# Performance work log

Hardware: AMD Instinct MI355X
Metric: run time of the kernel (lower is better)

Reference implementation:

```python
import jax, jax.numpy as jnp
import numpy as np
from math import sqrt

B, N, CS, H, D, K = 8, 256, 512, 8, 64, 32
NB = 2 * K + 1          # no_bins = 65
CT = 2048               # c_transition
INF = 1e9
WL = sqrt(0.5)          # w_L
EPS = 1e-5


def setup_inputs() -> dict:
    key = jax.random.key(0)
    ks = jax.random.split(key, 10)
    sc = 0.02
    return {
        "s": jax.random.normal(ks[0], (B, N, CS), jnp.float32),
        "masks": jnp.ones((B, N), jnp.bool_),
        "wq": jax.random.normal(ks[1], (CS, D * H), jnp.float32) * sc,
        "wk": jax.random.normal(ks[2], (CS, D * H), jnp.float32) * sc,
        "wv": jax.random.normal(ks[3], (CS, D * H), jnp.float32) * sc,
        "wb": jax.random.normal(ks[4], (NB, H), jnp.float32) * sc,
        "wo": jax.random.normal(ks[5], ((NB + D) * H, CS), jnp.float32) * sc,
        "bo": jnp.zeros((CS,), jnp.float32),
        "ln1_g": jnp.ones((CS,), jnp.float32),
        "ln1_b": jnp.zeros((CS,), jnp.float32),
        "w1": jax.random.normal(ks[6], (CS, CT), jnp.float32) * sc,
        "b1": jnp.zeros((CT,), jnp.float32),
        "w2": jax.random.normal(ks[7], (CT, CS), jnp.float32) * sc,
        "b2": jnp.zeros((CS,), jnp.float32),
        "ln2_g": jnp.ones((CS,), jnp.float32),
        "ln2_b": jnp.zeros((CS,), jnp.float32),
    }


def _layernorm(x, g, b):
    m = jnp.mean(x, -1, keepdims=True)
    v = jnp.var(x, -1, keepdims=True)
    return (x - m) * jax.lax.rsqrt(v + EPS) * g + b


def _heads(x):  # [B,N,D*H] -> [B,H,N,D]  (torch: reshape(B,N,D,H) then move H forward)
    return jnp.transpose(x.reshape(B, N, D, H), (0, 3, 1, 2))


def reference(s, masks, wq, wk, wv, wb, wo, bo, ln1_g, ln1_b, w1, b1, w2, b2, ln2_g, ln2_b):
    mf = masks.astype(s.dtype)                       # [B,N]
    sq = mf[:, :, None] * mf[:, None, :]             # [B,N,N]

    # relative position one-hot, clipped to [-K, K] -> [N,N,NB]
    r = jnp.arange(N)
    dmat = jnp.clip(r[:, None] - r[None, :], -K, K) + K
    relpos_base = jax.nn.one_hot(dmat, NB, dtype=s.dtype)
    relpos = relpos_base[None] * sq[..., None]       # [B,N,N,NB]

    b_bias = jnp.einsum('bijc,ch->bhij', relpos, wb)  # [B,H,N,N]

    q = _heads(s @ wq)                               # [B,H,N,D]
    k = _heads(s @ wk)
    v = _heads(s @ wv)

    logits = WL * (jnp.einsum('bhid,bhjd->bhij', q, k) / sqrt(D) + b_bias)
    logits = logits - INF * (1.0 - sq)[:, None]      # mask
    a = jax.nn.softmax(logits, axis=-1)              # [B,H,N,N]

    # pairwise aggregation and value aggregation (einsum avoids [B,H,N,N,NB] blowup)
    o_pair = jnp.einsum('bhij,bijc->bhic', a, relpos)  # [B,H,N,NB]
    o = jnp.einsum('bhij,bhjd->bhid', a, v)            # [B,H,N,D]

    op = jnp.transpose(o_pair, (0, 2, 1, 3)).reshape(B, N, H * NB)
    ov = jnp.transpose(o, (0, 2, 1, 3)).reshape(B, N, H * D)
    embd = jnp.concatenate([op, ov], axis=-1) @ wo + bo   # [B,N,CS]

    x = _layernorm(s + embd, ln1_g, ln1_b)
    ff = jax.nn.relu(x @ w1 + b1) @ w2 + b2
    x = _layernorm(x + ff, ln2_g, ln2_b)
    return x, a
```

## Files before the change

kernel.cpp:

```cpp
#include <hip/hip_runtime.h>
#include <hip/hip_bf16.h>
#include <cstdint>

#define B_ 8
#define N_ 256
#define CS_ 512
#define H_ 8
#define D_ 64
#define K_ 32
#define NB_ 65
#define CT_ 2048
#define WL_ 0.70710678118654752f

typedef __attribute__((ext_vector_type(8))) short bf16x8;
typedef __attribute__((ext_vector_type(4))) float f32x4;

#define GLOBAL_AS __attribute__((address_space(1)))
#define LDS_AS __attribute__((address_space(3)))

__device__ __forceinline__ void async16(void* lds, const void* g) {
  __builtin_amdgcn_global_load_lds((const GLOBAL_AS uint32_t*)g,
                                   (LDS_AS uint32_t*)lds, 16, 0, 0);
}

__device__ __forceinline__ ushort f2bf(float v) {
  __hip_bfloat16 hb = __float2bfloat16(v);
  return *(ushort*)&hb;
}

__device__ __forceinline__ float bf2f(ushort u) {
  union { uint32_t ui; float f; } cv; cv.ui = (uint32_t)u << 16;
  return cv.f;
}

__global__ __launch_bounds__(128, 2) void gemm_bf16(
    const ushort* __restrict__ A, const ushort* __restrict__ Bt,
    const float* __restrict__ bias, float* __restrict__ C,
    ushort* __restrict__ Cb, int M, int Nc, int Kd, int flags) {
  __shared__ ushort As[2][64 * 64];
  __shared__ ushort Bs[2][64 * 64];
  int tid = threadIdx.x;
  int bm = blockIdx.y * 64, bn = blockIdx.x * 64;
  int S = gridDim.z, z = blockIdx.z;
  int T = Kd >> 6;
  int it0 = (z * T) / S, it1 = ((z + 1) * T) / S;
  if (flags & 32) Cb += (size_t)z * M * Nc;
  int w = tid >> 6, l = tid & 63;
  int lm = l & 15, lq = l >> 4;
  int srow = tid >> 3;
  int sg = tid & 7;

  f32x4 acc[2][4];
#pragma unroll
  for (int i = 0; i < 2; ++i)
#pragma unroll
    for (int j = 0; j < 4; ++j) acc[i][j] = (f32x4){0.f, 0.f, 0.f, 0.f};

  {
    int k0 = it0 << 6;
#pragma unroll
    for (int r = 0; r < 4; ++r) {
      int row = r * 16 + srow;
      int gl = sg ^ (row & 7);
      async16(&As[0][row * 64 + sg * 8],
              A + (size_t)(bm + row) * Kd + k0 + gl * 8);
      async16(&Bs[0][row * 64 + sg * 8],
              Bt + (size_t)(bn + row) * Kd + k0 + gl * 8);
    }
  }
  for (int it = it0; it < it1; ++it) {
    int cur = (it - it0) & 1;
    __syncthreads();
    if (it + 1 < it1) {
      int nxt = cur ^ 1;
      int k0 = (it + 1) << 6;
#pragma unroll
      for (int r = 0; r < 4; ++r) {
        int row = r * 16 + srow;
        int gl = sg ^ (row & 7);
        async16(&As[nxt][row * 64 + sg * 8],
                A + (size_t)(bm + row) * Kd + k0 + gl * 8);
        async16(&Bs[nxt][row * 64 + sg * 8],
                Bt + (size_t)(bn + row) * Kd + k0 + gl * 8);
      }
    }
#pragma unroll
    for (int kk = 0; kk < 2; ++kk) {
      bf16x8 af[2], bfr[4];
#pragma unroll
      for (int i = 0; i < 2; ++i) {
        int ma = w * 32 + 16 * i + lm;
        af[i] = *(const bf16x8*)&As[cur][ma * 64 + ((kk * 4 + lq) ^ (ma & 7)) * 8];
      }
#pragma unroll
      for (int j = 0; j < 4; ++j) {
        int nb = 16 * j + lm;
        bfr[j] = *(const bf16x8*)&Bs[cur][nb * 64 + ((kk * 4 + lq) ^ (nb & 7)) * 8];
      }
#pragma unroll
      for (int i = 0; i < 2; ++i)
#pragma unroll
        for (int j = 0; j < 4; ++j)
          acc[i][j] = __builtin_amdgcn_mfma_f32_16x16x32_bf16(
              af[i], bfr[j], acc[i][j], 0, 0, 0);
    }
  }
  __syncthreads();

  int lr = l >> 3, lc = l & 7;
  ushort* Tb = &As[0][0] + w * 2048;

#pragma unroll
  for (int j = 0; j < 4; ++j) {
    float bv = ((flags & 1) && z == 0) ? bias[bn + 16 * j + lm] : 0.f;
#pragma unroll
    for (int i = 0; i < 2; ++i)
#pragma unroll
      for (int r = 0; r < 4; ++r) {
        float v = acc[i][j][r] + bv;
        if (flags & 2) v = fmaxf(v, 0.f);
        Tb[(16 * i + lq * 4 + r) * 64 + 16 * j + lm] = f2bf(v);
      }
  }
  __asm__ __volatile__("" ::: "memory");
#pragma unroll
  for (int p = 0; p < 4; ++p) {
    int rowL = p * 8 + lr;
    bf16x8 vv = *(const bf16x8*)&Tb[rowL * 64 + lc * 8];
    *(bf16x8*)(Cb + (size_t)(bm + w * 32 + rowL) * Nc + bn + lc * 8) = vv;
  }
}

__global__ __launch_bounds__(128, 2) void qkvT(
    const ushort* __restrict__ A, const ushort* __restrict__ Bt,
    ushort* __restrict__ Cb,
    const float* __restrict__ wo, const float* __restrict__ w1,
    const float* __restrict__ w2, ushort* __restrict__ wopT,
    ushort* __restrict__ w1T, ushort* __restrict__ w2T) {
  __shared__ __align__(16) ushort As[2][64 * 64];
  __shared__ ushort Bs[2][64 * 64];
  int blk = blockIdx.x, tid = threadIdx.x;

  if (blk >= 768) {
    float (*tile)[33] = (float(*)[33])&As[0][0];
    int t = blk - 768;
    const float* src; ushort* dst;
    int R, C, Kpad, tX, tIdx;
    if (t < 544)       { tIdx = t;        src = wo; dst = wopT; R = 1032; C = 512;  Kpad = 1088; tX = 16; }
    else if (t < 1568) { tIdx = t - 544;  src = w1; dst = w1T;  R = 512;  C = 2048; Kpad = 512;  tX = 64; }
    else               { tIdx = t - 1568; src = w2; dst = w2T;  R = 2048; C = 512;  Kpad = 2048; tX = 16; }
    int c0 = (tIdx % tX) * 32, r0 = (tIdx / tX) * 32;
    int tx = tid & 7, ty = tid >> 3;
#pragma unroll
    for (int yy = 0; yy < 32; yy += 16) {
      int r = r0 + yy + ty, c = c0 + tx * 4;
      float4 v = (r < R) ? *(const float4*)&src[(size_t)r * C + c]
                         : (float4){0.f, 0.f, 0.f, 0.f};
      tile[yy + ty][tx * 4 + 0] = v.x;
      tile[yy + ty][tx * 4 + 1] = v.y;
      tile[yy + ty][tx * 4 + 2] = v.z;
      tile[yy + ty][tx * 4 + 3] = v.w;
    }
    __syncthreads();
#pragma unroll
    for (int yy = 0; yy < 32; yy += 16) {
      int cc = c0 + yy + ty;
      int k = r0 + tx * 4;
      float a0 = tile[tx * 4 + 0][yy + ty];
      float a1 = tile[tx * 4 + 1][yy + ty];
      float a2 = tile[tx * 4 + 2][yy + ty];
      float a3 = tile[tx * 4 + 3][yy + ty];
      ushort pk[4] = {f2bf(a0), f2bf(a1), f2bf(a2), f2bf(a3)};
      *(uint2*)&dst[(size_t)cc * Kpad + k] = *(uint2*)pk;
    }
    return;
  }

  int bm = (blk / 24) * 64, bn = (blk % 24) * 64;
  const int Kd = 512, it1 = 8;
  int w = tid >> 6, l = tid & 63;
  int lm = l & 15, lq = l >> 4;
  int srow = tid >> 3;
  int sg = tid & 7;

  f32x4 acc[2][4];
#pragma unroll
  for (int i = 0; i < 2; ++i)
#pragma unroll
    for (int j = 0; j < 4; ++j) acc[i][j] = (f32x4){0.f, 0.f, 0.f, 0.f};

  {
#pragma unroll
    for (int r = 0; r < 4; ++r) {
      int row = r * 16 + srow;
      int gl = sg ^ (row & 7);
      async16(&As[0][row * 64 + sg * 8],
              A + (size_t)(bm + row) * Kd + gl * 8);
      async16(&Bs[0][row * 64 + sg * 8],
              Bt + (size_t)(bn + row) * Kd + gl * 8);
    }
  }
  for (int it = 0; it < it1; ++it) {
    int cur = it & 1;
    __syncthreads();
    if (it + 1 < it1) {
      int nxt = cur ^ 1;
      int k0 = (it + 1) << 6;
#pragma unroll
      for (int r = 0; r < 4; ++r) {
        int row = r * 16 + srow;
        int gl = sg ^ (row & 7);
        async16(&As[nxt][row * 64 + sg * 8],
                A + (size_t)(bm + row) * Kd + k0 + gl * 8);
        async16(&Bs[nxt][row * 64 + sg * 8],
                Bt + (size_t)(bn + row) * Kd + k0 + gl * 8);
      }
    }
#pragma unroll
    for (int kk = 0; kk < 2; ++kk) {
      bf16x8 af[2], bfr[4];
#pragma unroll
      for (int i = 0; i < 2; ++i) {
        int ma = w * 32 + 16 * i + lm;
        af[i] = *(const bf16x8*)&As[cur][ma * 64 + ((kk * 4 + lq) ^ (ma & 7)) * 8];
      }
#pragma unroll
      for (int j = 0; j < 4; ++j) {
        int nb = 16 * j + lm;
        bfr[j] = *(const bf16x8*)&Bs[cur][nb * 64 + ((kk * 4 + lq) ^ (nb & 7)) * 8];
      }
#pragma unroll
      for (int i = 0; i < 2; ++i)
#pragma unroll
        for (int j = 0; j < 4; ++j)
          acc[i][j] = __builtin_amdgcn_mfma_f32_16x16x32_bf16(
              af[i], bfr[j], acc[i][j], 0, 0, 0);
    }
  }
  __syncthreads();

  int lr = l >> 3, lc = l & 7;
  ushort* Tb = &As[0][0] + w * 2048;

  int which = bn >> 9;
  int hh = (bn & 511) >> 6;
  int b = bm >> 8, nn0 = bm & 255;
  if (which == 2) {
#pragma unroll
    for (int j = 0; j < 4; ++j)
#pragma unroll
      for (int i = 0; i < 2; ++i) {
        ushort pk[4];
#pragma unroll
        for (int r = 0; r < 4; ++r) pk[r] = f2bf(acc[i][j][r]);
        *(uint2*)&Tb[(16 * j + lm) * 32 + 16 * i + lq * 4] = *(uint2*)pk;
      }
  } else {
#pragma unroll
    for (int j = 0; j < 4; ++j)
#pragma unroll
      for (int i = 0; i < 2; ++i)
#pragma unroll
        for (int r = 0; r < 4; ++r)
          Tb[(16 * i + lq * 4 + r) * 64 + 16 * j + lm] = f2bf(acc[i][j][r]);
  }
  __asm__ __volatile__("" ::: "memory");
  ushort* dstb = Cb + (size_t)which * 1048576 + (size_t)(b * 8 + hh) * 16384;
  if (which == 2) {
    int vr = l >> 2, vc = l & 3;
#pragma unroll
    for (int p = 0; p < 4; ++p) {
      int rowL = p * 16 + vr;
      bf16x8 vv = *(const bf16x8*)&Tb[rowL * 32 + vc * 8];
      *(bf16x8*)(dstb + (size_t)rowL * 256 + nn0 + w * 32 + vc * 8) = vv;
    }
  } else {
#pragma unroll
    for (int p = 0; p < 4; ++p) {
      int rowL = p * 8 + lr;
      bf16x8 vv = *(const bf16x8*)&Tb[rowL * 64 + lc * 8];
      *(bf16x8*)(dstb + (size_t)(nn0 + w * 32 + rowL) * 64 + lc * 8) = vv;
    }
  }
}

__global__ __launch_bounds__(256) void prep_small(
    const float* __restrict__ s, __hip_bfloat16* __restrict__ s_bf,
    const float* __restrict__ wq, const float* __restrict__ wk,
    const float* __restrict__ wv, __hip_bfloat16* __restrict__ wqkvT) {
  int blk = blockIdx.x;
  if (blk < 512) {
    int i = blk * 256 + threadIdx.x;
    float4 a = ((const float4*)s)[i * 2];
    float4 c = ((const float4*)s)[i * 2 + 1];
    ushort pk[8] = {f2bf(a.x), f2bf(a.y), f2bf(a.z), f2bf(a.w),
                    f2bf(c.x), f2bf(c.y), f2bf(c.z), f2bf(c.w)};
    *(uint4*)&((ushort*)s_bf)[i * 8] = *(uint4*)pk;
    return;
  }
  int t = blk - 512;
  __shared__ float tile[32][33];
  int zz = t >> 8, tIdx = t & 255;
  const float* src = zz == 0 ? wq : zz == 1 ? wk : wv;
  int whichBase = zz * 512;
  int c0 = (tIdx & 15) * 32, r0 = (tIdx >> 4) * 32;
  int tx = threadIdx.x & 7, ty = threadIdx.x >> 3;
  {
    int r = r0 + ty, c = c0 + tx * 4;
    float4 v = *(const float4*)&src[(size_t)r * 512 + c];
    tile[ty][tx * 4 + 0] = v.x;
    tile[ty][tx * 4 + 1] = v.y;
    tile[ty][tx * 4 + 2] = v.z;
    tile[ty][tx * 4 + 3] = v.w;
  }
  __syncthreads();
  {
    int cc = c0 + ty;
    int k = r0 + tx * 4;
    float a0 = tile[tx * 4 + 0][ty];
    float a1 = tile[tx * 4 + 1][ty];
    float a2 = tile[tx * 4 + 2][ty];
    float a3 = tile[tx * 4 + 3][ty];
    int n = whichBase + (cc & 7) * 64 + (cc >> 3);
    ushort pk[4] = {f2bf(a0), f2bf(a1), f2bf(a2), f2bf(a3)};
    *(uint2*)&((ushort*)wqkvT)[(size_t)n * 512 + k] = *(uint2*)pk;
  }
}

__global__ __launch_bounds__(128) void attn_fused(
    const ushort* __restrict__ qh, const ushort* __restrict__ kh,
    const ushort* __restrict__ vT, const int* __restrict__ masks,
    const float* __restrict__ wb, float* __restrict__ a_out,
    ushort* __restrict__ cat) {
  int strip = blockIdx.x & 7, bh = blockIdx.x >> 3;
  int h = bh & 7, b = bh >> 3;
  __shared__ ushort Ks[256 * 64];
  __shared__ ushort Ps[32 * 64];
  __shared__ float wbs[NB_];
  __shared__ float mfj[256];
  int tid = threadIdx.x;
  int srow = tid >> 3, sg = tid & 7;
#pragma unroll
  for (int rr = 0; rr < 16; ++rr) {
    int row = rr * 16 + srow;
    int gl = sg ^ (row & 7);
    async16(&Ks[row * 64 + sg * 8],
            kh + ((size_t)bh * 256 + row) * 64 + gl * 8);
  }
  int w = tid >> 6, l = tid & 63, lm = l & 15, lq = l >> 4;
  bf16x8 qf[2];
  {
    const ushort* qrow =
        qh + ((size_t)bh * 256 + strip * 32 + w * 16 + lm) * 64 + lq * 8;
    qf[0] = *(const bf16x8*)qrow;
    qf[1] = *(const bf16x8*)(qrow + 32);
  }
  if (tid < NB_) wbs[tid] = wb[tid * H_ + h];
  mfj[tid]       = (masks[b * 256 + tid] != 0) ? 1.f : 0.f;
  mfj[tid + 128] = (masks[b * 256 + tid + 128] != 0) ? 1.f : 0.f;
  __syncthreads();

  f32x4 acc[16];
#pragma unroll
  for (int ct = 0; ct < 16; ++ct) {
    int krow = ct * 16 + lm;
    bf16x8 kf0 = *(const bf16x8*)&Ks[krow * 64 + ((lq) ^ (krow & 7)) * 8];
    bf16x8 kf1 = *(const bf16x8*)&Ks[krow * 64 + ((4 + lq) ^ (krow & 7)) * 8];
    f32x4 zf = (f32x4){0.f, 0.f, 0.f, 0.f};
    zf = __builtin_amdgcn_mfma_f32_16x16x32_bf16(qf[0], kf0, zf, 0, 0, 0);
    acc[ct] = __builtin_amdgcn_mfma_f32_16x16x32_bf16(qf[1], kf1, zf, 0, 0, 0);
  }
  int ibase = strip * 32 + w * 16 + lq * 4;
  float mfi[4];
#pragma unroll
  for (int r = 0; r < 4; ++r) mfi[r] = mfj[ibase + r];
#pragma unroll
  for (int ct = 0; ct < 16; ++ct) {
    int j = ct * 16 + lm;
    float mj = mfj[j];
#pragma unroll
    for (int r = 0; r < 4; ++r) {
      int i = ibase + r;
      int diff = i - j;
      int cb = diff < -K_ ? 0 : (diff > K_ ? 2 * K_ : diff + K_);
      float sq = mfi[r] * mj;
      acc[ct][r] = WL_ * (acc[ct][r] * 0.125f + wbs[cb] * sq) - 1e9f * (1.f - sq);
    }
  }
  float mx[4], sm[4];
#pragma unroll
  for (int r = 0; r < 4; ++r) {
    float m = acc[0][r];
#pragma unroll
    for (int ct = 1; ct < 16; ++ct) m = fmaxf(m, acc[ct][r]);
#pragma unroll
    for (int o = 1; o < 16; o <<= 1) m = fmaxf(m, __shfl_xor(m, o, 64));
    mx[r] = m;
  }
#pragma unroll
  for (int ct = 0; ct < 16; ++ct)
#pragma unroll
    for (int r = 0; r < 4; ++r) acc[ct][r] = __expf(acc[ct][r] - mx[r]);
#pragma unroll
  for (int r = 0; r < 4; ++r) {
    float s = 0.f;
#pragma unroll
    for (int ct = 0; ct < 16; ++ct) s += acc[ct][r];
#pragma unroll
    for (int o = 1; o < 16; o <<= 1) s += __shfl_xor(s, o, 64);
    sm[r] = 1.f / s;
  }
  float p0[4] = {0.f, 0.f, 0.f, 0.f}, p64[4] = {0.f, 0.f, 0.f, 0.f};
#pragma unroll
  for (int ct = 0; ct < 16; ++ct) {
    int j = ct * 16 + lm;
    float mj = mfj[j];
#pragma unroll
    for (int r = 0; r < 4; ++r) {
      int i = ibase + r;
      float aval = acc[ct][r] * sm[r];
      a_out[((size_t)bh * 256 + i) * 256 + j] = aval;
      float val = aval * mfi[r] * mj;
      int diff = i - j;
      if (diff <= -K_)      p0[r] += val;
      else if (diff >= K_)  p64[r] += val;
      else cat[((size_t)(b * 256 + i)) * 1088 + h * 65 + diff + K_] = f2bf(val);
    }
  }
#pragma unroll
  for (int r = 0; r < 4; ++r)
#pragma unroll
    for (int o = 1; o < 16; o <<= 1) {
      p0[r]  += __shfl_xor(p0[r], o, 64);
      p64[r] += __shfl_xor(p64[r], o, 64);
    }
  if (lm == 0) {
#pragma unroll
    for (int r = 0; r < 4; ++r) {
      int i = ibase + r;
      cat[((size_t)(b * 256 + i)) * 1088 + h * 65 + 0]      = f2bf(p0[r]);
      cat[((size_t)(b * 256 + i)) * 1088 + h * 65 + 2 * K_] = f2bf(p64[r]);
    }
  }
#pragma unroll
  for (int r = 0; r < 4; ++r) {
    int i = ibase + r;
#pragma unroll
    for (int t = 0; t < 4; ++t) {
      int c = 1 + lm + 16 * t;
      if (c < 64) {
        int j = i - c + K_;
        if (j < 0 || j > 255)
          cat[((size_t)(b * 256 + i)) * 1088 + h * 65 + c] = 0;
      }
    }
  }
  if (h == 0) {
    for (int idx = tid; idx < 32 * 56; idx += 128) {
      int r = idx / 56, c = 1032 + (idx - r * 56);
      cat[((size_t)(b * 256 + strip * 32 + r)) * 1088 + c] = 0;
    }
  }
  f32x4 acc2[4];
#pragma unroll
  for (int nt = 0; nt < 4; ++nt) acc2[nt] = (f32x4){0.f, 0.f, 0.f, 0.f};
  const ushort* vbase = vT + (size_t)bh * 16384;
#pragma unroll
  for (int qt = 0; qt < 4; ++qt) {
    bf16x8 vf0[4], vf1[4];
#pragma unroll
    for (int nt = 0; nt < 4; ++nt) {
      const ushort* vrow = vbase + (size_t)(nt * 16 + lm) * 256 + qt * 64 + lq * 8;
      vf0[nt] = *(const bf16x8*)vrow;
      vf1[nt] = *(const bf16x8*)(vrow + 32);
    }
#pragma unroll
    for (int ctl = 0; ctl < 4; ++ctl) {
      int ct = qt * 4 + ctl;
#pragma unroll
      for (int r = 0; r < 4; ++r) {
        int rowl = w * 16 + lq * 4 + r;
        int g = ctl * 2 + (lm >> 3);
        Ps[rowl * 64 + ((g ^ (rowl & 7)) << 3) + (lm & 7)] =
            f2bf(acc[ct][r] * sm[r]);
      }
    }
    int prow = w * 16 + lm;
#pragma unroll
    for (int kst = 0; kst < 2; ++kst) {
      bf16x8 af = *(const bf16x8*)&Ps[prow * 64 + (((kst * 4 + lq) ^ (prow & 7)) << 3)];
#pragma unroll
      for (int nt = 0; nt < 4; ++nt)
        acc2[nt] = __builtin_amdgcn_mfma_f32_16x16x32_bf16(
            af, kst ? vf1[nt] : vf0[nt], acc2[nt], 0, 0, 0);
    }
  }
#pragma unroll
  for (int nt = 0; nt < 4; ++nt) {
    int d = nt * 16 + lm;
#pragma unroll
    for (int r = 0; r < 4; ++r) {
      int i = ibase + r;
      cat[((size_t)(b * 256 + i)) * 1088 + 520 + h * 64 + d] = f2bf(acc2[nt][r]);
    }
  }
}

__global__ __launch_bounds__(128) void ln_sum(
    const float* __restrict__ x1, const ushort* __restrict__ xp,
    int S, int stride, const float* __restrict__ g,
    const float* __restrict__ bta, float* __restrict__ out,
    __hip_bfloat16* __restrict__ out_bf) {
  __shared__ float redA[2], redB[2];
  int row = blockIdx.x, tid = threadIdx.x;
  size_t base = (size_t)row * 512;
  float4 v = *(const float4*)(x1 + base + tid * 4);
  for (int s = 0; s < S; ++s) {
    uint2 p = *(const uint2*)(xp + (size_t)s * stride + base + tid * 4);
    v.x += bf2f((ushort)(p.x & 0xffff));
    v.y += bf2f((ushort)(p.x >> 16));
    v.z += bf2f((ushort)(p.y & 0xffff));
    v.w += bf2f((ushort)(p.y >> 16));
  }
  float su = v.x + v.y + v.z + v.w;
  float sq = v.x * v.x + v.y * v.y + v.z * v.z + v.w * v.w;
#pragma unroll
  for (int o = 32; o > 0; o >>= 1) {
    su += __shfl_xor(su, o, 64);
    sq += __shfl_xor(sq, o, 64);
  }
  int w = tid >> 6;
  if ((tid & 63) == 0) { redA[w] = su; redB[w] = sq; }
  __syncthreads();
  su = redA[0] + redA[1]; sq = redB[0] + redB[1];
  float mean = su * (1.f / 512.f);
  float var = sq * (1.f / 512.f) - mean * mean;
  float inv = rsqrtf(var + 1e-5f);
  float4 gv = *(const float4*)(g + tid * 4);
  float4 bv = *(const float4*)(bta + tid * 4);
  float4 o4;
  o4.x = (v.x - mean) * inv * gv.x + bv.x;
  o4.y = (v.y - mean) * inv * gv.y + bv.y;
  o4.z = (v.z - mean) * inv * gv.z + bv.z;
  o4.w = (v.w - mean) * inv * gv.w + bv.w;
  *(float4*)(out + base + tid * 4) = o4;
  if (out_bf) {
    ushort pk[4] = {f2bf(o4.x), f2bf(o4.y), f2bf(o4.z), f2bf(o4.w)};
    *(uint2*)&((ushort*)out_bf)[base + tid * 4] = *(uint2*)pk;
  }
}

extern "C" void kernel_launch(void* const* d_in, const int* in_sizes, int n_in,
                              void* d_out, int out_size, void* d_ws, size_t ws_size,
                              hipStream_t stream) {
  const float* s     = (const float*)d_in[0];
  const int*   masks = (const int*)d_in[1];
  const float* wq = (const float*)d_in[2];
  const float* wk = (const float*)d_in[3];
  const float* wv = (const float*)d_in[4];
  const float* wb = (const float*)d_in[5];
  const float* wo = (const float*)d_in[6];
  const float* bo = (const float*)d_in[7];
  const float* ln1_g = (const float*)d_in[8];
  const float* ln1_b = (const float*)d_in[9];
  const float* w1 = (const float*)d_in[10];
  const float* b1 = (const float*)d_in[11];
  const float* w2 = (const float*)d_in[12];
  const float* b2 = (const float*)d_in[13];
  const float* ln2_g = (const float*)d_in[14];
  const float* ln2_b = (const float*)d_in[15];

  float* out_x = (float*)d_out;
  float* out_a = out_x + 1048576;

  float* ws = (float*)d_ws;
  ushort* embd_part = (ushort*)(ws + 0);
  float* xbuf       = ws + 4194304;
  ushort* ff_part   = (ushort*)(ws + 5242880);
  ushort* qkv_bf    = (ushort*)(ws + 9437184);
  ushort* q_bf = qkv_bf;
  ushort* k_bf = qkv_bf + 1048576;
  ushort* v_bf = qkv_bf + 2097152;
  ushort* cat_bf = (ushort*)(ws + 10223616);
  __hip_bfloat16* h_bf  = (__hip_bfloat16*)(ws + 11337728);
  __hip_bfloat16* s_bf  = (__hip_bfloat16*)(ws + 13434880);
  __hip_bfloat16* x_bf  = (__hip_bfloat16*)(ws + 13959168);
  __hip_bfloat16* wqkvT = (__hip_bfloat16*)(ws + 14483456);
  ushort* wopT  = (ushort*)(ws + 14876672);
  ushort* w1T   = (ushort*)(ws + 15155200);
  ushort* w2T   = (ushort*)(ws + 15679488);

  dim3 blkg(128);
  prep_small<<<dim3(1280), dim3(256), 0, stream>>>(s, s_bf, wq, wk, wv, wqkvT);
  qkvT<<<dim3(3360), blkg, 0, stream>>>(
      (const ushort*)s_bf, (const ushort*)wqkvT, qkv_bf,
      wo, w1, w2, wopT, w1T, w2T);
  attn_fused<<<dim3(512), blkg, 0, stream>>>(q_bf, k_bf, v_bf, masks, wb,
                                             out_a, cat_bf);
  gemm_bf16<<<dim3(8, 32, 2), blkg, 0, stream>>>(
      cat_bf, wopT, bo, nullptr, embd_part, 2048, 512, 1088, 1 | 4 | 32);
  ln_sum<<<dim3(2048), blkg, 0, stream>>>(s, embd_part, 2, 1048576,
                                          ln1_g, ln1_b, xbuf, x_bf);
  gemm_bf16<<<dim3(32, 32, 1), blkg, 0, stream>>>(
      (const ushort*)x_bf, w1T, b1, nullptr, (ushort*)h_bf,
      2048, 2048, 512, 1 | 2 | 4);
  gemm_bf16<<<dim3(8, 32, 2), blkg, 0, stream>>>(
      (const ushort*)h_bf, w2T, b2, nullptr, ff_part,
      2048, 512, 2048, 1 | 4 | 32);
  ln_sum<<<dim3(2048), blkg, 0, stream>>>(xbuf, ff_part, 2, 1048576,
                                          ln2_g, ln2_b, out_x, nullptr);
}
```

Measured before the change: 169.3 us.

## Add 64x128 GEMM tile for FFN up-projection and batch rows in LayerNorm

Adds a gemm128 kernel that computes 64x128 output tiles, with each wave owning 64 columns, and uses it for the x@w1 ReLU GEMM so each A tile is reused across twice as many columns. ln_sum now handles four rows per block with 512 blocks, which amortises the gamma/beta loads and the launch across rows. The gemm_bf16 calls drop flag bit 4, whose meaning is not visible in the shown code. The larger accumulator tile raises register pressure and halves the block count of the w1 GEMM, which may hurt occupancy.

```diff
diff --git a/kernel.cpp b/kernel.cpp
--- a/kernel.cpp
+++ b/kernel.cpp
@@ -131,6 +131,106 @@
   }
 }
 
+__global__ __launch_bounds__(128, 2) void gemm128(
+    const ushort* __restrict__ A, const ushort* __restrict__ Bt,
+    const float* __restrict__ bias, ushort* __restrict__ Cb,
+    int M, int Nc, int Kd, int flags) {
+  __shared__ ushort As[2][64 * 64];
+  __shared__ ushort Bs[2][128 * 64];
+  int tid = threadIdx.x;
+  int bm = blockIdx.y * 64, bn = blockIdx.x * 128;
+  int T = Kd >> 6;
+  int w = tid >> 6, l = tid & 63;
+  int lm = l & 15, lq = l >> 4;
+  int srow = tid >> 3;
+  int sg = tid & 7;
+
+  f32x4 acc[4][4];
+#pragma unroll
+  for (int i = 0; i < 4; ++i)
+#pragma unroll
+    for (int j = 0; j < 4; ++j) acc[i][j] = (f32x4){0.f, 0.f, 0.f, 0.f};
+
+  {
+#pragma unroll
+    for (int r = 0; r < 4; ++r) {
+      int row = r * 16 + srow;
+      int gl = sg ^ (row & 7);
+      async16(&As[0][row * 64 + sg * 8], A + (size_t)(bm + row) * Kd + gl * 8);
+    }
+#pragma unroll
+    for (int r = 0; r < 8; ++r) {
+      int row = r * 16 + srow;
+      int gl = sg ^ (row & 7);
+      async16(&Bs[0][row * 64 + sg * 8], Bt + (size_t)(bn + row) * Kd + gl * 8);
+    }
+  }
+  for (int it = 0; it < T; ++it) {
+    int cur = it & 1;
+    __syncthreads();
+    if (it + 1 < T) {
+      int nxt = cur ^ 1;
+      int k0 = (it + 1) << 6;
+#pragma unroll
+      for (int r = 0; r < 4; ++r) {
+        int row = r * 16 + srow;
+        int gl = sg ^ (row & 7);
+        async16(&As[nxt][row * 64 + sg * 8],
+                A + (size_t)(bm + row) * Kd + k0 + gl * 8);
+      }
+#pragma unroll
+      for (int r = 0; r < 8; ++r) {
+        int row = r * 16 + srow;
+        int gl = sg ^ (row & 7);
+        async16(&Bs[nxt][row * 64 + sg * 8],
+                Bt + (size_t)(bn + row) * Kd + k0 + gl * 8);
+      }
+    }
+#pragma unroll
+    for (int kk = 0; kk < 2; ++kk) {
+      bf16x8 af[4], bfr[4];
+#pragma unroll
+      for (int i = 0; i < 4; ++i) {
+        int ma = 16 * i + lm;
+        af[i] = *(const bf16x8*)&As[cur][ma * 64 + ((kk * 4 + lq) ^ (ma & 7)) * 8];
+        int nb = w * 64 + 16 * i + lm;
+        bfr[i] = *(const bf16x8*)&Bs[cur][nb * 64 + ((kk * 4 + lq) ^ (nb & 7)) * 8];
+      }
+#pragma unroll
+      for (int i = 0; i < 4; ++i)
+#pragma unroll
+        for (int j = 0; j < 4; ++j)
+          acc[i][j] = __builtin_amdgcn_mfma_f32_16x16x32_bf16(
+              af[i], bfr[j], acc[i][j], 0, 0, 0);
+    }
+  }
+  __syncthreads();
+
+  int bcol0 = bn + w * 64;
+  int lr = l >> 3, lc = l & 7;
+  ushort* Tb = &Bs[0][w * 4096];
+
+#pragma unroll
+  for (int j = 0; j < 4; ++j) {
+    float bv = (flags & 1) ? bias[bcol0 + 16 * j + lm] : 0.f;
+#pragma unroll
+    for (int i = 0; i < 4; ++i)
+#pragma unroll
+      for (int r = 0; r < 4; ++r) {
+        float v = acc[i][j][r] + bv;
+        if (flags & 2) v = fmaxf(v, 0.f);
+        Tb[(16 * i + lq * 4 + r) * 64 + 16 * j + lm] = f2bf(v);
+      }
+  }
+  __asm__ __volatile__("" ::: "memory");
+#pragma unroll
+  for (int p = 0; p < 8; ++p) {
+    int rowL = p * 8 + lr;
+    bf16x8 vv = *(const bf16x8*)&Tb[rowL * 64 + lc * 8];
+    *(bf16x8*)(Cb + (size_t)(bm + rowL) * Nc + bcol0 + lc * 8) = vv;
+  }
+}
+
 __global__ __launch_bounds__(128, 2) void qkvT(
     const ushort* __restrict__ A, const ushort* __restrict__ Bt,
     ushort* __restrict__ Cb,
@@ -512,41 +612,46 @@
     const float* __restrict__ bta, float* __restrict__ out,
     __hip_bfloat16* __restrict__ out_bf) {
   __shared__ float redA[2], redB[2];
-  int row = blockIdx.x, tid = threadIdx.x;
-  size_t base = (size_t)row * 512;
-  float4 v = *(const float4*)(x1 + base + tid * 4);
-  for (int s = 0; s < S; ++s) {
-    uint2 p = *(const uint2*)(xp + (size_t)s * stride + base + tid * 4);
-    v.x += bf2f((ushort)(p.x & 0xffff));
-    v.y += bf2f((ushort)(p.x >> 16));
-    v.z += bf2f((ushort)(p.y & 0xffff));
-    v.w += bf2f((ushort)(p.y >> 16));
-  }
-  float su = v.x + v.y + v.z + v.w;
-  float sq = v.x * v.x + v.y * v.y + v.z * v.z + v.w * v.w;
-#pragma unroll
-  for (int o = 32; o > 0; o >>= 1) {
-    su += __shfl_xor(su, o, 64);
-    sq += __shfl_xor(sq, o, 64);
-  }
+  int tid = threadIdx.x;
   int w = tid >> 6;
-  if ((tid & 63) == 0) { redA[w] = su; redB[w] = sq; }
-  __syncthreads();
-  su = redA[0] + redA[1]; sq = redB[0] + redB[1];
-  float mean = su * (1.f / 512.f);
-  float var = sq * (1.f / 512.f) - mean * mean;
-  float inv = rsqrtf(var + 1e-5f);
   float4 gv = *(const float4*)(g + tid * 4);
   float4 bv = *(const float4*)(bta + tid * 4);
-  float4 o4;
-  o4.x = (v.x - mean) * inv * gv.x + bv.x;
-  o4.y = (v.y - mean) * inv * gv.y + bv.y;
-  o4.z = (v.z - mean) * inv * gv.z + bv.z;
-  o4.w = (v.w - mean) * inv * gv.w + bv.w;
-  *(float4*)(out + base + tid * 4) = o4;
-  if (out_bf) {
-    ushort pk[4] = {f2bf(o4.x), f2bf(o4.y), f2bf(o4.z), f2bf(o4.w)};
-    *(uint2*)&((ushort*)out_bf)[base + tid * 4] = *(uint2*)pk;
+#pragma unroll
+  for (int rr = 0; rr < 4; ++rr) {
+    int row = blockIdx.x + rr * 512;
+    size_t base = (size_t)row * 512;
+    float4 v = *(const float4*)(x1 + base + tid * 4);
+    for (int s = 0; s < S; ++s) {
+      uint2 p = *(const uint2*)(xp + (size_t)s * stride + base + tid * 4);
+      v.x += bf2f((ushort)(p.x & 0xffff));
+      v.y += bf2f((ushort)(p.x >> 16));
+      v.z += bf2f((ushort)(p.y & 0xffff));
+      v.w += bf2f((ushort)(p.y >> 16));
+    }
+    float su = v.x + v.y + v.z + v.w;
+    float sq = v.x * v.x + v.y * v.y + v.z * v.z + v.w * v.w;
+#pragma unroll
+    for (int o = 32; o > 0; o >>= 1) {
+      su += __shfl_xor(su, o, 64);
+      sq += __shfl_xor(sq, o, 64);
+    }
+    if ((tid & 63) == 0) { redA[w] = su; redB[w] = sq; }
+    __syncthreads();
+    su = redA[0] + redA[1]; sq = redB[0] + redB[1];
+    float mean = su * (1.f / 512.f);
+    float var = sq * (1.f / 512.f) - mean * mean;
+    float inv = rsqrtf(var + 1e-5f);
+    float4 o4;
+    o4.x = (v.x - mean) * inv * gv.x + bv.x;
+    o4.y = (v.y - mean) * inv * gv.y + bv.y;
+    o4.z = (v.z - mean) * inv * gv.z + bv.z;
+    o4.w = (v.w - mean) * inv * gv.w + bv.w;
+    *(float4*)(out + base + tid * 4) = o4;
+    if (out_bf) {
+      ushort pk[4] = {f2bf(o4.x), f2bf(o4.y), f2bf(o4.z), f2bf(o4.w)};
+      *(uint2*)&((ushort*)out_bf)[base + tid * 4] = *(uint2*)pk;
+    }
+    __syncthreads();
   }
 }
 
@@ -598,15 +703,14 @@
   attn_fused<<<dim3(512), blkg, 0, stream>>>(q_bf, k_bf, v_bf, masks, wb,
                                              out_a, cat_bf);
   gemm_bf16<<<dim3(8, 32, 2), blkg, 0, stream>>>(
-      cat_bf, wopT, bo, nullptr, embd_part, 2048, 512, 1088, 1 | 4 | 32);
-  ln_sum<<<dim3(2048), blkg, 0, stream>>>(s, embd_part, 2, 1048576,
-                                          ln1_g, ln1_b, xbuf, x_bf);
-  gemm_bf16<<<dim3(32, 32, 1), blkg, 0, stream>>>(
-      (const ushort*)x_bf, w1T, b1, nullptr, (ushort*)h_bf,
-      2048, 2048, 512, 1 | 2 | 4);
+      cat_bf, wopT, bo, nullptr, embd_part, 2048, 512, 1088, 1 | 32);
+  ln_sum<<<dim3(512), blkg, 0, stream>>>(s, embd_part, 2, 1048576,
+                                         ln1_g, ln1_b, xbuf, x_bf);
+  gemm128<<<dim3(16, 32, 1), blkg, 0, stream>>>(
+      (const ushort*)x_bf, w1T, b1, (ushort*)h_bf, 2048, 2048, 512, 1 | 2);
   gemm_bf16<<<dim3(8, 32, 2), blkg, 0, stream>>>(
       (const ushort*)h_bf, w2T, b2, nullptr, ff_part,
-      2048, 512, 2048, 1 | 4 | 32);
-  ln_sum<<<dim3(2048), blkg, 0, stream>>>(xbuf, ff_part, 2, 1048576,
-                                          ln2_g, ln2_b, out_x, nullptr);
-}
+      2048, 512, 2048, 1 | 32);
+  ln_sum<<<dim3(512), blkg, 0, stream>>>(xbuf, ff_part, 2, 1048576,
+                                         ln2_g, ln2_b, out_x, nullptr);
+}
```

Result: slower. 175.0 us (+3.3%).
